# Performance work log

Measured on AMD Instinct MI355X. Metric: run time of the kernel, lower is better.

## Reference

```python
import jax, jax.numpy as jnp
import numpy as np
from jax import lax

D_MODEL = 1024
D_STATE = 16
D_CONV = 4
D_INNER = 2 * D_MODEL
B_SZ = 2
L_SEQ = 1024
EPS = 1e-5


def setup_inputs() -> dict:
    key = jax.random.key(0)
    ks = jax.random.split(key, 8)
    s = lambda k, shape, scale: jax.random.normal(k, shape, jnp.float32) * scale
    return {
        "x": jax.random.normal(ks[0], (B_SZ, L_SEQ, D_MODEL), jnp.float32),
        "norm_w": jnp.ones((D_MODEL,), jnp.float32),
        "norm_b": jnp.zeros((D_MODEL,), jnp.float32),
        "in_proj_w": s(ks[1], (2 * D_INNER, D_MODEL), 0.02),
        "in_proj_b": jnp.zeros((2 * D_INNER,), jnp.float32),
        "conv_w": s(ks[2], (D_INNER, 1, D_CONV), 0.1),   # torch Conv1d weight (out, in/groups, k)
        "conv_b": jnp.zeros((D_INNER,), jnp.float32),
        "x_proj_w": s(ks[3], (2 * D_STATE, D_INNER), 0.02),
        "x_proj_b": jnp.zeros((2 * D_STATE,), jnp.float32),
        "dt_proj_w": s(ks[4], (D_INNER, D_INNER), 0.02),
        "dt_proj_b": jnp.zeros((D_INNER,), jnp.float32),
        "A_log": s(ks[5], (D_INNER, D_STATE), 1.0),
        "D_param": jnp.ones((D_INNER,), jnp.float32),
        "out_proj_w": s(ks[6], (D_MODEL, D_INNER), 0.02),
        "out_proj_b": jnp.zeros((D_MODEL,), jnp.float32),
    }


def _layernorm(x, w, b):
    mu = jnp.mean(x, axis=-1, keepdims=True)
    var = jnp.mean(jnp.square(x - mu), axis=-1, keepdims=True)
    return (x - mu) * lax.rsqrt(var + EPS) * w + b


def _silu(x):
    return x * jax.nn.sigmoid(x)


def _selective_scan(u, delta, A, B_ssm, C_ssm):
    # u, delta: (B, L, d_inner); A: (d_inner, d_state); B_ssm, C_ssm: (B, L, d_state)
    dA = jnp.exp(delta[..., None] * A)                    # (B, L, d_inner, d_state)
    dBu = (delta * u)[..., None] * B_ssm[:, :, None, :]   # (B, L, d_inner, d_state)
    # time-major for scan
    dA_t = jnp.moveaxis(dA, 1, 0)
    dBu_t = jnp.moveaxis(dBu, 1, 0)
    C_t = jnp.moveaxis(C_ssm, 1, 0)

    def step(h, inp):
        dA_i, dBu_i, c_i = inp
        h = dA_i * h + dBu_i                              # (B, d_inner, d_state)
        y = jnp.einsum('bds,bs->bd', h, c_i)
        return h, y

    h0 = jnp.zeros((u.shape[0], u.shape[2], A.shape[1]), u.dtype)
    _, ys = lax.scan(step, h0, (dA_t, dBu_t, C_t))
    return jnp.moveaxis(ys, 0, 1)                         # (B, L, d_inner)


def reference(x, norm_w, norm_b, in_proj_w, in_proj_b, conv_w, conv_b,
              x_proj_w, x_proj_b, dt_proj_w, dt_proj_b, A_log, D_param,
              out_proj_w, out_proj_b):
    residual = x
    xn = _layernorm(x, norm_w, norm_b)
    xz = xn @ in_proj_w.T + in_proj_b                     # (B, L, 2*d_inner)
    xc, z = jnp.split(xz, 2, axis=-1)
    # depthwise causal conv1d (torch pads both sides d_conv-1 then slices :L == left pad)
    kern = jnp.transpose(conv_w, (2, 1, 0))               # (k, 1, d_inner) for 'LIO'
    xc = lax.conv_general_dilated(
        xc, kern, window_strides=(1,), padding=[(D_CONV - 1, 0)],
        dimension_numbers=('NLC', 'LIO', 'NLC'), feature_group_count=D_INNER) + conv_b
    u = _silu(xc)
    x_db = u @ x_proj_w.T + x_proj_b                      # (B, L, 2*d_state)
    B_ssm, C_ssm = jnp.split(x_db, 2, axis=-1)
    delta = jax.nn.softplus(u @ dt_proj_w.T + dt_proj_b)  # (B, L, d_inner)
    A = -jnp.exp(A_log)
    y = _selective_scan(u, delta, A, B_ssm, C_ssm)
    y = y + u * D_param
    y = y * _silu(z)
    out = y @ out_proj_w.T + out_proj_b
    return residual + out
```

## Files before the change

kernel.cpp:

```cpp
#include <hip/hip_runtime.h>

#define DM   1024
#define DI   2048
#define LSEQ 1024
#define BSZ  2
#define MROWS (BSZ*LSEQ)
#define NCH   (BSZ*DI)
#define SCHUNK 32
#define STEPS  32
#define PLANE  (NCH*16)

typedef __attribute__((ext_vector_type(4)))  float  f32x4;
typedef __attribute__((ext_vector_type(8)))  __bf16 bf16x8;
typedef __attribute__((ext_vector_type(8)))  unsigned short u16x8;

__device__ __forceinline__ unsigned short f2bf(float f) {
  union { float f; unsigned int u; } v; v.f = f;
  unsigned int u = v.u;
  unsigned int r = (u + 0x7fffu + ((u >> 16) & 1u)) >> 16;
  return (unsigned short)r;
}
__device__ __forceinline__ float bf2f(unsigned short h) {
  union { unsigned int u; float f; } v; v.u = (unsigned int)h << 16; return v.f;
}

__device__ __forceinline__ void load_lds16(const void* g, void* l) {
  __builtin_amdgcn_global_load_lds((const __attribute__((address_space(1))) void*)g,
                                   (__attribute__((address_space(3))) void*)l, 16, 0, 0);
}

__global__ __launch_bounds__(256) void prep(
    const float* __restrict__ x, const float* __restrict__ nw, const float* __restrict__ nb,
    unsigned short* __restrict__ xn_bf,
    const float* __restrict__ s0, unsigned short* __restrict__ d0,
    const float* __restrict__ s1, unsigned short* __restrict__ d1,
    const float* __restrict__ s2, unsigned short* __restrict__ d2,
    const float* __restrict__ s3, unsigned short* __restrict__ d3)
{
  int tid = threadIdx.x;
  if (blockIdx.x < MROWS) {
    int row = blockIdx.x;
    const float4* xr = (const float4*)(x + (size_t)row * DM);
    float4 v = xr[tid];
    float s  = v.x + v.y + v.z + v.w;
    float s2v = v.x*v.x + v.y*v.y + v.z*v.z + v.w*v.w;
    #pragma unroll
    for (int off = 32; off > 0; off >>= 1) { s += __shfl_down(s, off); s2v += __shfl_down(s2v, off); }
    __shared__ float ss[4], sq[4];
    if ((tid & 63) == 0) { ss[tid >> 6] = s; sq[tid >> 6] = s2v; }
    __syncthreads();
    float mean = (ss[0]+ss[1]+ss[2]+ss[3]) * (1.0f/DM);
    float var  = (sq[0]+sq[1]+sq[2]+sq[3]) * (1.0f/DM) - mean*mean;
    float rs = rsqrtf(var + 1e-5f);
    float4 wv = ((const float4*)nw)[tid];
    float4 bv = ((const float4*)nb)[tid];
    ushort4 o;
    o.x = f2bf((v.x-mean)*rs*wv.x + bv.x);
    o.y = f2bf((v.y-mean)*rs*wv.y + bv.y);
    o.z = f2bf((v.z-mean)*rs*wv.z + bv.z);
    o.w = f2bf((v.w-mean)*rs*wv.w + bv.w);
    ((ushort4*)(xn_bf + (size_t)row * DM))[tid] = o;
  } else {
    const int N0 = 4096*1024/4, N1 = 2048*2048/4, N2 = 1024*2048/4, N3 = 32*2048/4;
    int i = (blockIdx.x - MROWS) * 256 + tid;
    int stride = (gridDim.x - MROWS) * 256;
    int total = N0 + N1 + N2 + N3;
    for (; i < total; i += stride) {
      const float* s; unsigned short* d; int j = i;
      if (j < N0) { s = s0; d = d0; }
      else if ((j -= N0) < N1) { s = s1; d = d1; }
      else if ((j -= N1) < N2) { s = s2; d = d2; }
      else { j -= N2; s = s3; d = d3; }
      float4 v = ((const float4*)s)[j];
      ushort4 o;
      o.x = f2bf(v.x); o.y = f2bf(v.y); o.z = f2bf(v.z); o.w = f2bf(v.w);
      ((ushort4*)d)[j] = o;
    }
  }
}

template<int EPI, int MV, int NV, typename OT>
__global__ __launch_bounds__(256) void gemm_bt(
    const unsigned short* __restrict__ A, const unsigned short* __restrict__ Bw,
    const float* __restrict__ bias, const float* __restrict__ resid,
    OT* __restrict__ C, int N, int K)
{
  constexpr int BM = MV * 32;
  constexpr int BN = NV * 32;
  constexpr int VM = MV + NV;
  __shared__ unsigned short As[2][BM*64];
  __shared__ unsigned short Bs[2][BN*64];
  const int tid  = threadIdx.x;
  const int lane = tid & 63;
  const int w    = tid >> 6;

  const int nbx = gridDim.x;
  const int nwg = gridDim.x * gridDim.y;
  int wg  = blockIdx.y * nbx + blockIdx.x;
  int swz = (wg & 7) * (nwg >> 3) + (wg >> 3);
  const int m0 = (swz / nbx) * BM;
  const int n0 = (swz % nbx) * BN;

  const int wm = w >> 1, wn = w & 1;
  const int r16 = lane & 15;
  const int kg  = lane >> 4;

  const int srow = tid >> 3;
  const int kl   = (tid & 7) ^ (srow & 7);
  const unsigned short* gaBase = A  + (size_t)(m0 + srow) * K + kl * 8;
  const unsigned short* gbBase = Bw + (size_t)(n0 + srow) * K + kl * 8;

  f32x4 acc[MV][NV] = {};

  auto stage = [&](int buf, int kt) {
    const unsigned short* ga = gaBase + kt;
    #pragma unroll
    for (int p = 0; p < MV; ++p)
      load_lds16(ga + (size_t)(32*p)*K, (char*)As[buf] + p*4096 + tid*16);
    const unsigned short* gb = gbBase + kt;
    #pragma unroll
    for (int p = 0; p < NV; ++p)
      load_lds16(gb + (size_t)(32*p)*K, (char*)Bs[buf] + p*4096 + tid*16);
  };

  stage(0, 0);
  stage(1, 64);

  int cur = 0;
  for (int kt = 0; kt < K; kt += 64) {
    if (kt + 64 < K) asm volatile("s_waitcnt vmcnt(%0)" :: "i"(VM) : "memory");
    else             asm volatile("s_waitcnt vmcnt(0)" ::: "memory");
    __builtin_amdgcn_s_barrier();

    bf16x8 av[2][MV], bv[2][NV];
    #pragma unroll
    for (int kk = 0; kk < 2; ++kk) {
      const int phys = (kk*4 + kg) ^ (r16 & 7);
      #pragma unroll
      for (int i = 0; i < MV; ++i)
        av[kk][i] = *(const bf16x8*)((const char*)As[cur] + (wm*(MV*16) + i*16 + r16)*128 + phys*16);
      #pragma unroll
      for (int j = 0; j < NV; ++j)
        bv[kk][j] = *(const bf16x8*)((const char*)Bs[cur] + (wn*(NV*16) + j*16 + r16)*128 + phys*16);
    }
    #pragma unroll
    for (int kk = 0; kk < 2; ++kk)
      #pragma unroll
      for (int i = 0; i < MV; ++i)
        #pragma unroll
        for (int j = 0; j < NV; ++j)
          acc[i][j] = __builtin_amdgcn_mfma_f32_16x16x32_bf16(av[kk][i], bv[kk][j], acc[i][j], 0, 0, 0);

    asm volatile("s_waitcnt lgkmcnt(0)" ::: "memory");
    __builtin_amdgcn_s_barrier();
    if (kt + 128 < K) stage(cur, kt + 128);
    cur ^= 1;
  }

  #pragma unroll
  for (int i = 0; i < MV; ++i) {
    int rbase = m0 + wm*(MV*16) + i*16 + kg*4;
    #pragma unroll
    for (int j = 0; j < NV; ++j) {
      int col = n0 + wn*(NV*16) + j*16 + r16;
      float bcol = bias[col];
      #pragma unroll
      for (int r = 0; r < 4; ++r) {
        int row = rbase + r;
        float v = acc[i][j][r] + bcol;
        if (EPI == 1) v = (v > 20.f) ? v : log1pf(__expf(v));
        if (EPI == 2) v += resid[(size_t)row * N + col];
        if constexpr (sizeof(OT) == 2) C[(size_t)row * N + col] = f2bf(v);
        else                           C[(size_t)row * N + col] = v;
      }
    }
  }
}

__global__ __launch_bounds__(256) void conv_silu(const unsigned short* __restrict__ xz,
    const float* __restrict__ cw, const float* __restrict__ cb,
    unsigned short* __restrict__ u_bf)
{
  int t8 = blockIdx.x * 256 + threadIdx.x;
  int d8 = (t8 << 3) & (DI-1);
  int m  = t8 >> 8;
  int l  = m & (LSEQ-1);
  const unsigned short* base = xz + (size_t)m * (2*DI) + d8;
  u16x8 r0 = *(const u16x8*)base;
  u16x8 r1 = (l >= 1) ? *(const u16x8*)(base - (2*DI))   : u16x8{};
  u16x8 r2 = (l >= 2) ? *(const u16x8*)(base - 2*(2*DI)) : u16x8{};
  u16x8 r3 = (l >= 3) ? *(const u16x8*)(base - 3*(2*DI)) : u16x8{};
  float4 cb0 = *(const float4*)(cb + d8);
  float4 cb1 = *(const float4*)(cb + d8 + 4);
  u16x8 o;
  #pragma unroll
  for (int e = 0; e < 8; ++e) {
    int d = d8 + e;
    float w0 = cw[d*4+0], w1 = cw[d*4+1], w2 = cw[d*4+2], w3 = cw[d*4+3];
    float acc = (e < 4) ? ((const float*)&cb0)[e] : ((const float*)&cb1)[e-4];
    acc += w3 * bf2f(r0[e]);
    if (l >= 1) acc += w2 * bf2f(r1[e]);
    if (l >= 2) acc += w1 * bf2f(r2[e]);
    if (l >= 3) acc += w0 * bf2f(r3[e]);
    float s = acc / (1.f + __expf(-acc));
    o[e] = f2bf(s);
  }
  *(u16x8*)(u_bf + (size_t)m * DI + d8) = o;
}

__global__ __launch_bounds__(64) void xproj_mfma(const unsigned short* __restrict__ u_bf,
    const unsigned short* __restrict__ wx, const float* __restrict__ bias,
    float* __restrict__ xdb)
{
  int lane = threadIdx.x;
  int m0 = blockIdx.x * 16;
  int r16 = lane & 15, kg = lane >> 4;
  f32x4 acc0 = {}, acc1 = {};
  const unsigned short* ap  = u_bf + (size_t)(m0 + r16) * DI + kg*8;
  const unsigned short* b0p = wx   + (size_t)r16        * DI + kg*8;
  const unsigned short* b1p = wx   + (size_t)(16 + r16) * DI + kg*8;
  #pragma unroll 4
  for (int kt = 0; kt < DI; kt += 32) {
    bf16x8 a  = *(const bf16x8*)(ap  + kt);
    bf16x8 b0 = *(const bf16x8*)(b0p + kt);
    bf16x8 b1 = *(const bf16x8*)(b1p + kt);
    acc0 = __builtin_amdgcn_mfma_f32_16x16x32_bf16(a, b0, acc0, 0, 0, 0);
    acc1 = __builtin_amdgcn_mfma_f32_16x16x32_bf16(a, b1, acc1, 0, 0, 0);
  }
  #pragma unroll
  for (int r = 0; r < 4; ++r) {
    int row = m0 + kg*4 + r;
    xdb[row*32 + r16]      = acc0[r] + bias[r16];
    xdb[row*32 + 16 + r16] = acc1[r] + bias[16 + r16];
  }
}

__global__ __launch_bounds__(256) void scan_p1(const unsigned short* __restrict__ delta,
    const unsigned short* __restrict__ u, const float* __restrict__ xdb,
    const float* __restrict__ A_log, float* __restrict__ agg_a, float* __restrict__ agg_b)
{
  int tid = threadIdx.x;
  int sh  = tid & 3;
  int ch  = blockIdx.x * 64 + (tid >> 2);
  int c   = blockIdx.y;
  int b = ch >> 11, d = ch & (DI-1);
  float Ads[4];
  {
    f32x4 Ar = *(const f32x4*)(A_log + d*16 + sh*4);
    #pragma unroll
    for (int s = 0; s < 4; ++s) Ads[s] = -__expf(Ar[s]);
  }
  float a[4] = {1.f,1.f,1.f,1.f}, bb[4] = {0.f,0.f,0.f,0.f};
  int row0 = b * LSEQ + c * STEPS;
  const unsigned short* dp = delta + (size_t)row0 * DI + d;
  const unsigned short* up = u     + (size_t)row0 * DI + d;
  #pragma unroll 4
  for (int t = 0; t < STEPS; ++t) {
    float dl = bf2f(dp[t*DI]);
    float uu = bf2f(up[t*DI]);
    f32x4 Bv = *(const f32x4*)(xdb + (size_t)(row0 + t) * 32 + sh*4);
    float dlu = dl * uu;
    #pragma unroll
    for (int s = 0; s < 4; ++s) {
      float dA = __expf(dl * Ads[s]);
      bb[s] = fmaf(dA, bb[s], dlu * Bv[s]);
      a[s] *= dA;
    }
  }
  int idx = c*PLANE + ch*16 + sh*4;
  f32x4 av, bv;
  #pragma unroll
  for (int s = 0; s < 4; ++s) { av[s] = a[s]; bv[s] = bb[s]; }
  *(f32x4*)(agg_a + idx) = av;
  *(f32x4*)(agg_b + idx) = bv;
}

__global__ __launch_bounds__(256) void scan_p2(const float* __restrict__ agg_a,
    const float* __restrict__ agg_b, float* __restrict__ hinit)
{
  int idx = blockIdx.x * 256 + threadIdx.x;
  float h = 0.f;
  #pragma unroll
  for (int c = 0; c < SCHUNK; ++c) {
    hinit[c*PLANE + idx] = h;
    h = fmaf(agg_a[c*PLANE + idx], h, agg_b[c*PLANE + idx]);
  }
}

__global__ __launch_bounds__(256) void scan_p3(const unsigned short* __restrict__ delta,
    const unsigned short* __restrict__ u, const float* __restrict__ xdb,
    const float* __restrict__ A_log, const float* __restrict__ Dp,
    const unsigned short* __restrict__ xz, const float* __restrict__ hinit,
    unsigned short* __restrict__ y_bf)
{
  int tid = threadIdx.x;
  int sh  = tid & 3;
  int ch  = blockIdx.x * 64 + (tid >> 2);
  int c   = blockIdx.y;
  int b = ch >> 11, d = ch & (DI-1);
  float Ads[4];
  {
    f32x4 Ar = *(const f32x4*)(A_log + d*16 + sh*4);
    #pragma unroll
    for (int s = 0; s < 4; ++s) Ads[s] = -__expf(Ar[s]);
  }
  float h[4];
  {
    f32x4 hv = *(const f32x4*)(hinit + c*PLANE + ch*16 + sh*4);
    #pragma unroll
    for (int s = 0; s < 4; ++s) h[s] = hv[s];
  }
  float Dd = Dp[d];
  int row0 = b * LSEQ + c * STEPS;
  const unsigned short* dp = delta + (size_t)row0 * DI + d;
  const unsigned short* up = u     + (size_t)row0 * DI + d;
  const unsigned short* zp = xz    + (size_t)row0 * (2*DI) + DI + d;
  unsigned short* yp = y_bf + (size_t)row0 * DI + d;
  #pragma unroll 2
  for (int t = 0; t < STEPS; ++t) {
    float dl = bf2f(dp[t*DI]);
    float uu = bf2f(up[t*DI]);
    const float* xr = xdb + (size_t)(row0 + t) * 32 + sh*4;
    f32x4 Bv = *(const f32x4*)xr;
    f32x4 Cv = *(const f32x4*)(xr + 16);
    float dlu = dl * uu;
    float y = 0.f;
    #pragma unroll
    for (int s = 0; s < 4; ++s) {
      float dA = __expf(dl * Ads[s]);
      h[s] = fmaf(dA, h[s], dlu * Bv[s]);
      y = fmaf(h[s], Cv[s], y);
    }
    y += __shfl_xor(y, 1);
    y += __shfl_xor(y, 2);
    if (sh == 0) {
      float zz = bf2f(zp[t*(2*DI)]);
      float yv = y + uu * Dd;
      yv *= zz / (1.f + __expf(-zz));
      yp[t*DI] = f2bf(yv);
    }
  }
}

extern "C" void kernel_launch(void* const* d_in, const int* in_sizes, int n_in,
                              void* d_out, int out_size, void* d_ws, size_t ws_size,
                              hipStream_t stream)
{
  (void)in_sizes; (void)n_in; (void)out_size;
  const float* x      = (const float*)d_in[0];
  const float* norm_w = (const float*)d_in[1];
  const float* norm_b = (const float*)d_in[2];
  const float* in_w   = (const float*)d_in[3];
  const float* in_b   = (const float*)d_in[4];
  const float* conv_w = (const float*)d_in[5];
  const float* conv_b = (const float*)d_in[6];
  const float* xp_w   = (const float*)d_in[7];
  const float* xp_b   = (const float*)d_in[8];
  const float* dt_w   = (const float*)d_in[9];
  const float* dt_b   = (const float*)d_in[10];
  const float* A_log  = (const float*)d_in[11];
  const float* D_par  = (const float*)d_in[12];
  const float* out_w  = (const float*)d_in[13];
  const float* out_b  = (const float*)d_in[14];
  float* out = (float*)d_out;

  char* p = (char*)d_ws;
  unsigned short* xn_bf = (unsigned short*)p;  p += 2048ull*1024*2;
  unsigned short* w_in  = (unsigned short*)p;  p += 4096ull*1024*2;
  unsigned short* w_dt  = (unsigned short*)p;  p += 2048ull*2048*2;
  unsigned short* w_out = (unsigned short*)p;  p += 1024ull*2048*2;
  unsigned short* wx_bf = (unsigned short*)p;  p += 32ull*2048*2;
  unsigned short* xz    = (unsigned short*)p;  p += 2048ull*4096*2;
  unsigned short* u_bf  = (unsigned short*)p;  p += 2048ull*2048*2;
  float*          xdb   = (float*)p;           p += 2048ull*32*4;
  unsigned short* delta = (unsigned short*)p;  p += 2048ull*2048*2;
  unsigned short* y_bf  = (unsigned short*)p;  p += 2048ull*2048*2;
  float*          hinit = (float*)p;           p += (size_t)PLANE*SCHUNK*4;
  if ((size_t)(p - (char*)d_ws) > ws_size) return;

  float* agg_a = (float*)w_in;
  float* agg_b = (float*)w_dt;

  prep<<<MROWS + 2048, 256, 0, stream>>>(x, norm_w, norm_b, xn_bf,
                                         in_w, w_in, dt_w, w_dt, out_w, w_out, xp_w, wx_bf);

  gemm_bt<0, 4, 2, unsigned short><<<dim3(4096/64, MROWS/128), 256, 0, stream>>>(xn_bf, w_in, in_b, nullptr, xz, 4096, 1024);
  conv_silu<<<(MROWS*DI)/(256*8), 256, 0, stream>>>(xz, conv_w, conv_b, u_bf);
  xproj_mfma<<<MROWS/16, 64, 0, stream>>>(u_bf, wx_bf, xp_b, xdb);
  gemm_bt<1, 4, 2, unsigned short><<<dim3(2048/64, MROWS/128), 256, 0, stream>>>(u_bf, w_dt, dt_b, nullptr, delta, 2048, 2048);

  scan_p1<<<dim3(NCH/64, SCHUNK), 256, 0, stream>>>(delta, u_bf, xdb, A_log, agg_a, agg_b);
  scan_p2<<<PLANE/256, 256, 0, stream>>>(agg_a, agg_b, hinit);
  scan_p3<<<dim3(NCH/64, SCHUNK), 256, 0, stream>>>(delta, u_bf, xdb, A_log, D_par, xz, hinit, y_bf);

  gemm_bt<2, 2, 2, float><<<dim3(1024/64, MROWS/64), 256, 0, stream>>>(y_bf, w_out, out_b, x, out, 1024, 2048);
}
```

Before: 202.3 us.

## Split-K the out_proj GEMM and reduce partials with residual and bias

Adds an EPI==3 mode to gemm_bt that splits K into two halves across blockIdx.z and writes fp32 partials into reused weight scratch buffers. A new reduce_k kernel then sums the two partials with the bias and the residual x. The aim is more workgroups for the output projection, so the GPU's CUs are better occupied. The cost is extra fp32 partial traffic and one more kernel launch.

```diff
diff --git a/kernel.cpp b/kernel.cpp
--- a/kernel.cpp
+++ b/kernel.cpp
@@ -94,6 +94,9 @@
   const int lane = tid & 63;
   const int w    = tid >> 6;
 
+  const int KS = (EPI == 3) ? (K >> 1) : K;
+  const int k0 = (EPI == 3) ? blockIdx.z * KS : 0;
+
   const int nbx = gridDim.x;
   const int nwg = gridDim.x * gridDim.y;
   int wg  = blockIdx.y * nbx + blockIdx.x;
@@ -107,8 +110,8 @@
 
   const int srow = tid >> 3;
   const int kl   = (tid & 7) ^ (srow & 7);
-  const unsigned short* gaBase = A  + (size_t)(m0 + srow) * K + kl * 8;
-  const unsigned short* gbBase = Bw + (size_t)(n0 + srow) * K + kl * 8;
+  const unsigned short* gaBase = A  + (size_t)(m0 + srow) * K + k0 + kl * 8;
+  const unsigned short* gbBase = Bw + (size_t)(n0 + srow) * K + k0 + kl * 8;
 
   f32x4 acc[MV][NV] = {};
 
@@ -127,9 +130,9 @@
   stage(1, 64);
 
   int cur = 0;
-  for (int kt = 0; kt < K; kt += 64) {
-    if (kt + 64 < K) asm volatile("s_waitcnt vmcnt(%0)" :: "i"(VM) : "memory");
-    else             asm volatile("s_waitcnt vmcnt(0)" ::: "memory");
+  for (int kt = 0; kt < KS; kt += 64) {
+    if (kt + 64 < KS) asm volatile("s_waitcnt vmcnt(%0)" :: "i"(VM) : "memory");
+    else              asm volatile("s_waitcnt vmcnt(0)" ::: "memory");
     __builtin_amdgcn_s_barrier();
 
     bf16x8 av[2][MV], bv[2][NV];
@@ -153,9 +156,12 @@
 
     asm volatile("s_waitcnt lgkmcnt(0)" ::: "memory");
     __builtin_amdgcn_s_barrier();
-    if (kt + 128 < K) stage(cur, kt + 128);
+    if (kt + 128 < KS) stage(cur, kt + 128);
     cur ^= 1;
   }
+
+  OT* Cb = C;
+  if constexpr (EPI == 3) Cb = C + (size_t)blockIdx.z * MROWS * N;
 
   #pragma unroll
   for (int i = 0; i < MV; ++i) {
@@ -163,18 +169,36 @@
     #pragma unroll
     for (int j = 0; j < NV; ++j) {
       int col = n0 + wn*(NV*16) + j*16 + r16;
-      float bcol = bias[col];
+      float bcol = (EPI == 3) ? 0.f : bias[col];
       #pragma unroll
       for (int r = 0; r < 4; ++r) {
         int row = rbase + r;
         float v = acc[i][j][r] + bcol;
         if (EPI == 1) v = (v > 20.f) ? v : log1pf(__expf(v));
         if (EPI == 2) v += resid[(size_t)row * N + col];
-        if constexpr (sizeof(OT) == 2) C[(size_t)row * N + col] = f2bf(v);
-        else                           C[(size_t)row * N + col] = v;
+        if constexpr (sizeof(OT) == 2) Cb[(size_t)row * N + col] = f2bf(v);
+        else                           Cb[(size_t)row * N + col] = v;
       }
     }
   }
+}
+
+__global__ __launch_bounds__(256) void reduce_k(const float* __restrict__ p0,
+    const float* __restrict__ p1, const float* __restrict__ x,
+    const float* __restrict__ bias, float* __restrict__ out)
+{
+  int i = blockIdx.x * 256 + threadIdx.x;
+  float4 a  = ((const float4*)p0)[i];
+  float4 b  = ((const float4*)p1)[i];
+  float4 xr = ((const float4*)x)[i];
+  int col4 = (i & (DM/4 - 1)) * 4;
+  float4 bs = *(const float4*)(bias + col4);
+  float4 o;
+  o.x = xr.x + bs.x + a.x + b.x;
+  o.y = xr.y + bs.y + a.y + b.y;
+  o.z = xr.z + bs.z + a.z + b.z;
+  o.w = xr.w + bs.w + a.w + b.w;
+  ((float4*)out)[i] = o;
 }
 
 __global__ __launch_bounds__(256) void conv_silu(const unsigned short* __restrict__ xz,
@@ -380,6 +404,10 @@
 
   float* agg_a = (float*)w_in;
   float* agg_b = (float*)w_dt;
+  float* partK = (float*)w_in;
+  float* part0 = (float*)w_in;
+  float* part1 = (float*)w_dt;
+  (void)partK;
 
   prep<<<MROWS + 2048, 256, 0, stream>>>(x, norm_w, norm_b, xn_bf,
                                          in_w, w_in, dt_w, w_dt, out_w, w_out, xp_w, wx_bf);
@@ -393,5 +421,6 @@
   scan_p2<<<PLANE/256, 256, 0, stream>>>(agg_a, agg_b, hinit);
   scan_p3<<<dim3(NCH/64, SCHUNK), 256, 0, stream>>>(delta, u_bf, xdb, A_log, D_par, xz, hinit, y_bf);
 
-  gemm_bt<2, 2, 2, float><<<dim3(1024/64, MROWS/64), 256, 0, stream>>>(y_bf, w_out, out_b, x, out, 1024, 2048);
-}
+  gemm_bt<3, 2, 2, float><<<dim3(1024/64, MROWS/64, 2), 256, 0, stream>>>(y_bf, w_out, out_b, nullptr, part0, 1024, 2048);
+  reduce_k<<<(MROWS*DM)/(4*256), 256, 0, stream>>>(part0, part1, x, out_b, out);
+}
```

Result: no change. 201.3 us (-0.5%).
